# Optimization experiments

Measured on AMD Instinct MI355X. Metric: run time of the kernel, lower is better.

The kernel has to match this reference:

```python
import jax, jax.numpy as jnp
import numpy as np

N_NODES = 50000
N_EDGES = 800000
IN_DIM = 256
HID = [256, 128]
NEG_SLOPE = 0.01  # F.leaky_relu default


def setup_inputs() -> dict:
    key = jax.random.key(0)
    ks = jax.random.split(key, 8)
    x = jax.random.normal(ks[0], (N_NODES, IN_DIM), dtype=jnp.float32)
    w1 = jax.random.normal(ks[1], (IN_DIM, HID[0]), dtype=jnp.float32) * (1.0 / np.sqrt(IN_DIM))
    b1 = jnp.zeros((HID[0],), dtype=jnp.float32)
    w2 = jax.random.normal(ks[2], (HID[0], HID[1]), dtype=jnp.float32) * (1.0 / np.sqrt(HID[0]))
    b2 = jnp.zeros((HID[1],), dtype=jnp.float32)
    src = jax.random.randint(ks[3], (N_EDGES,), 0, N_NODES, dtype=jnp.int32)
    dst = jax.random.randint(ks[4], (N_EDGES,), 0, N_NODES, dtype=jnp.int32)
    edge_weight = jax.random.uniform(ks[5], (N_EDGES,), dtype=jnp.float32)
    return {"x": x, "w1": w1, "b1": b1, "w2": w2, "b2": b2,
            "src": src, "dst": dst, "edge_weight": edge_weight}


def _gcn_layer(h, w, b, src, dst, ew, n_nodes):
    # GraphConvolution: support = h @ W ; out = spmm(adj, support) + b
    support = h @ w                              # [N, d_out]
    msg = support[src] * ew[:, None]             # [E, d_out] gather + scale
    agg = jax.ops.segment_sum(msg, dst, num_segments=n_nodes)  # [N, d_out]
    return agg + b


def reference(x, w1, b1, w2, b2, src, dst, edge_weight):
    # layer 1: GCN -> leaky_relu -> dropout(eval: identity)
    h = _gcn_layer(x, w1, b1, src, dst, edge_weight, N_NODES)
    h = jax.nn.leaky_relu(h, NEG_SLOPE)
    # layer 2
    h = _gcn_layer(h, w2, b2, src, dst, edge_weight, N_NODES)
    h = jax.nn.leaky_relu(h, NEG_SLOPE)
    return h
```

## Files before the change

kernel.cpp:

```cpp
#include <hip/hip_runtime.h>

#define NEG_SLOPE 0.01f

constexpr int N_NODES_C = 50000;
constexpr int N_EDGES_C = 800000;
constexpr int M_PAD = 50048;

typedef short bf16x8 __attribute__((ext_vector_type(8)));
typedef float f32x4 __attribute__((ext_vector_type(4)));

__device__ inline unsigned short f2bf(float f) {
  unsigned int u = __float_as_uint(f);
  u += 0x7FFF + ((u >> 16) & 1);
  return (unsigned short)(u >> 16);
}
__device__ inline float bf2f(unsigned int h16) {
  return __uint_as_float(h16 << 16);
}

constexpr int NB_CONVX = (M_PAD * 32) / 256;
constexpr int NB_W1 = (256 * 256) / 256;
constexpr int NB_W2 = (256 * 128) / 256;
constexpr int NB_HIST = N_EDGES_C / 256;
constexpr int NB_PRE = NB_CONVX + NB_W1 + NB_W2 + NB_HIST;

__global__ __launch_bounds__(256) void pre_kernel(
    const float* __restrict__ x, const float* __restrict__ w1,
    const float* __restrict__ w2, const int* __restrict__ dst,
    unsigned short* __restrict__ xb, unsigned short* __restrict__ w1T,
    unsigned short* __restrict__ w2T, int* __restrict__ counts) {
  const int bx = blockIdx.x;
  const int tid = threadIdx.x;
  if (bx < NB_CONVX) {
    int idx = bx * 256 + tid;
    int row = idx >> 5;
    int c8 = (idx & 31) << 3;
    uint4 v;
    if (row < N_NODES_C) {
      const float4* p = (const float4*)(x + (size_t)row * 256 + c8);
      float4 a = p[0], b = p[1];
      v.x = f2bf(a.x) | ((unsigned)f2bf(a.y) << 16);
      v.y = f2bf(a.z) | ((unsigned)f2bf(a.w) << 16);
      v.z = f2bf(b.x) | ((unsigned)f2bf(b.y) << 16);
      v.w = f2bf(b.z) | ((unsigned)f2bf(b.w) << 16);
    } else {
      v = make_uint4(0, 0, 0, 0);
    }
    *(uint4*)(xb + (size_t)row * 256 + c8) = v;
  } else if (bx < NB_CONVX + NB_W1) {
    int idx = (bx - NB_CONVX) * 256 + tid;
    int n = idx >> 8, k = idx & 255;
    w1T[idx] = f2bf(w1[(size_t)k * 256 + n]);
  } else if (bx < NB_CONVX + NB_W1 + NB_W2) {
    int idx = (bx - NB_CONVX - NB_W1) * 256 + tid;
    int n = idx >> 8, k = idx & 255;
    w2T[idx] = f2bf(w2[(size_t)k * 128 + n]);
  } else {
    int e = (bx - NB_CONVX - NB_W1 - NB_W2) * 256 + tid;
    atomicAdd(&counts[dst[e]], 1);
  }
}

constexpr int N_SCAN_BLKS = (N_NODES_C + 255) / 256;

__global__ __launch_bounds__(256) void scan_phase_a(const int* __restrict__ counts,
                                                    int* __restrict__ partial,
                                                    int* __restrict__ blk_sums) {
  __shared__ int s[256];
  const int t = threadIdx.x;
  const int i = blockIdx.x * 256 + t;
  const int v = (i < N_NODES_C) ? counts[i] : 0;
  s[t] = v;
  __syncthreads();
  for (int off = 1; off < 256; off <<= 1) {
    int u = (t >= off) ? s[t - off] : 0;
    __syncthreads();
    s[t] += u;
    __syncthreads();
  }
  if (i < N_NODES_C) partial[i] = s[t] - v;
  if (t == 255) blk_sums[blockIdx.x] = s[255];
}

__global__ __launch_bounds__(256) void scan_phase_b(const int* __restrict__ blk_sums,
                                                    int* __restrict__ blk_off) {
  __shared__ int s[256];
  const int t = threadIdx.x;
  const int v = (t < N_SCAN_BLKS) ? blk_sums[t] : 0;
  s[t] = v;
  __syncthreads();
  for (int off = 1; off < 256; off <<= 1) {
    int u = (t >= off) ? s[t - off] : 0;
    __syncthreads();
    s[t] += u;
    __syncthreads();
  }
  if (t < N_SCAN_BLKS) blk_off[t] = s[t] - v;
}

__global__ __launch_bounds__(256) void scan_phase_c(const int* __restrict__ partial,
                                                    const int* __restrict__ blk_off,
                                                    int* __restrict__ row_ptr,
                                                    int* __restrict__ cursor) {
  const int i = blockIdx.x * 256 + threadIdx.x;
  if (i < N_NODES_C) {
    const int r = partial[i] + blk_off[blockIdx.x];
    row_ptr[i] = r;
    cursor[i] = r;
  }
  if (i == 0) row_ptr[N_NODES_C] = N_EDGES_C;
}

__global__ __launch_bounds__(256) void fill_kernel(const int* __restrict__ src,
                                                   const int* __restrict__ dst,
                                                   const float* __restrict__ ew,
                                                   int* __restrict__ cursor,
                                                   uint2* __restrict__ s_meta) {
  int e = blockIdx.x * 256 + threadIdx.x;
  if (e < N_EDGES_C) {
    int p = atomicAdd(&cursor[dst[e]], 1);
    uint2 m;
    m.x = (unsigned)src[e];
    m.y = __float_as_uint(ew[e]);
    s_meta[p] = m;
  }
}


#define GLOAD_LDS16(g, l)                                              \
  __builtin_amdgcn_global_load_lds(                                    \
      (__attribute__((address_space(1))) void*)(g),                    \
      (__attribute__((address_space(3))) void*)(l), 16, 0, 0)

__global__ __launch_bounds__(256) void gemm_bf16_kernel(
    const unsigned short* __restrict__ A,
    const unsigned short* __restrict__ BT,
    unsigned short* __restrict__ C,
    int N) {
  constexpr int K = 256;
  __shared__ short Asm[128 * 32];
  __shared__ short Bsm[128 * 32];
  const int tid = threadIdx.x;
  const int lane = tid & 63, wave = tid >> 6;
  const int wm = wave & 1, wn = wave >> 1;
  const int row0 = blockIdx.y * 128, col0 = blockIdx.x * 128;

  const int ch0 = wave * 2, ch1 = wave * 2 + 1;
  const int o0 = ch0 * 512 + lane * 8;
  const int o1 = ch1 * 512 + lane * 8;
  const int r0 = o0 >> 5, c0 = o0 & 31;
  const int r1 = o1 >> 5, c1 = o1 & 31;

  f32x4 acc[4][4] = {};

  for (int k0 = 0; k0 < K; k0 += 32) {
    GLOAD_LDS16(A + (size_t)(row0 + r0) * K + k0 + c0, &Asm[ch0 * 512]);
    GLOAD_LDS16(A + (size_t)(row0 + r1) * K + k0 + c1, &Asm[ch1 * 512]);
    GLOAD_LDS16(BT + (size_t)(col0 + r0) * K + k0 + c0, &Bsm[ch0 * 512]);
    GLOAD_LDS16(BT + (size_t)(col0 + r1) * K + k0 + c1, &Bsm[ch1 * 512]);
    __builtin_amdgcn_s_waitcnt(0);
    __syncthreads();

    bf16x8 af[4], bf[4];
#pragma unroll
    for (int mt = 0; mt < 4; ++mt)
      af[mt] = *(const bf16x8*)&Asm[(wm * 64 + mt * 16 + (lane & 15)) * 32 + (lane >> 4) * 8];
#pragma unroll
    for (int nt = 0; nt < 4; ++nt)
      bf[nt] = *(const bf16x8*)&Bsm[(wn * 64 + nt * 16 + (lane & 15)) * 32 + (lane >> 4) * 8];
#pragma unroll
    for (int mt = 0; mt < 4; ++mt)
#pragma unroll
      for (int nt = 0; nt < 4; ++nt)
        acc[mt][nt] = __builtin_amdgcn_mfma_f32_16x16x32_bf16(af[mt], bf[nt], acc[mt][nt], 0, 0, 0);
    __syncthreads();
  }

  const int cl = lane & 15, rq = (lane >> 4) * 4;
#pragma unroll
  for (int mt = 0; mt < 4; ++mt) {
    const int rbase = row0 + wm * 64 + mt * 16 + rq;
#pragma unroll
    for (int nt = 0; nt < 4; ++nt) {
      const int col = col0 + wn * 64 + nt * 16 + cl;
      const size_t sbase = ((size_t)(col >> 5) * M_PAD) * 32 + (col & 31);
#pragma unroll
      for (int i = 0; i < 4; ++i)
        C[sbase + (size_t)(rbase + i) * 32] = f2bf(acc[mt][nt][i]);
    }
  }
}


__device__ inline void fma8(float* acc, uint4 v, float wt) {
  acc[0] += bf2f(v.x & 0xffffu) * wt;
  acc[1] += bf2f(v.x >> 16) * wt;
  acc[2] += bf2f(v.y & 0xffffu) * wt;
  acc[3] += bf2f(v.y >> 16) * wt;
  acc[4] += bf2f(v.z & 0xffffu) * wt;
  acc[5] += bf2f(v.z >> 16) * wt;
  acc[6] += bf2f(v.w & 0xffffu) * wt;
  acc[7] += bf2f(v.w >> 16) * wt;
}

template <int NSLICE, int OUT_D, bool OUT_BF16>
__global__ __launch_bounds__(256) void agg_quad_kernel(
    const unsigned short* __restrict__ supS,
    const uint2* __restrict__ s_meta, const int* __restrict__ row_ptr,
    const float* __restrict__ bias, unsigned short* __restrict__ out_bf,
    float* __restrict__ out_f, int n_total) {
  const int bx = blockIdx.x;
  const int slice = bx & (NSLICE - 1);
  const int group = bx / NSLICE;
  const int tid = threadIdx.x;
  const int quad = tid >> 2;
  const int dimg = tid & 3;
  const int n = group * 64 + quad;
  if (n >= n_total) return;
  const bool valid = n < N_NODES_C;
  const unsigned short* tab = supS + (size_t)slice * M_PAD * 32;

  float acc[8] = {};
  if (valid) {
    int j = row_ptr[n];
    const int end = row_ptr[n + 1];
    for (; j + 2 <= end; j += 2) {
      uint2 m0 = s_meta[j];
      uint2 m1 = s_meta[j + 1];
      uint4 v0 = *(const uint4*)(tab + m0.x * 32 + dimg * 8);
      uint4 v1 = *(const uint4*)(tab + m1.x * 32 + dimg * 8);
      fma8(acc, v0, __uint_as_float(m0.y));
      fma8(acc, v1, __uint_as_float(m1.y));
    }
    if (j < end) {
      uint2 m0 = s_meta[j];
      uint4 v0 = *(const uint4*)(tab + m0.x * 32 + dimg * 8);
      fma8(acc, v0, __uint_as_float(m0.y));
    }
  }

  const int dbase = slice * 32 + dimg * 8;
  if (OUT_BF16) {
    unsigned short o[8];
#pragma unroll
    for (int j = 0; j < 8; ++j) {
      float v = acc[j] + bias[dbase + j];
      v = v >= 0.f ? v : NEG_SLOPE * v;
      o[j] = f2bf(v);
    }
    uint4 pk;
    pk.x = o[0] | ((unsigned)o[1] << 16);
    pk.y = o[2] | ((unsigned)o[3] << 16);
    pk.z = o[4] | ((unsigned)o[5] << 16);
    pk.w = o[6] | ((unsigned)o[7] << 16);
    *(uint4*)(out_bf + (size_t)n * OUT_D + dbase) = pk;
  } else if (valid) {
    float r[8];
#pragma unroll
    for (int j = 0; j < 8; ++j) {
      float v = acc[j] + bias[dbase + j];
      r[j] = v >= 0.f ? v : NEG_SLOPE * v;
    }
    *(float4*)(out_f + (size_t)n * OUT_D + dbase) = make_float4(r[0], r[1], r[2], r[3]);
    *(float4*)(out_f + (size_t)n * OUT_D + dbase + 4) = make_float4(r[4], r[5], r[6], r[7]);
  }
}


extern "C" void kernel_launch(void* const* d_in, const int* in_sizes, int n_in,
                              void* d_out, int out_size, void* d_ws, size_t ws_size,
                              hipStream_t stream) {
  const float* x  = (const float*)d_in[0];
  const float* w1 = (const float*)d_in[1];
  const float* b1 = (const float*)d_in[2];
  const float* w2 = (const float*)d_in[3];
  const float* b2 = (const float*)d_in[4];
  const int*   src = (const int*)d_in[5];
  const int*   dst = (const int*)d_in[6];
  const float* ew  = (const float*)d_in[7];
  float* out = (float*)d_out;

  unsigned short* xb   = (unsigned short*)d_ws;
  unsigned short* a2b  = xb + (size_t)M_PAD * 256;
  unsigned short* sup1 = a2b + (size_t)M_PAD * 256;
  unsigned short* sup2 = sup1 + (size_t)M_PAD * 256;
  unsigned short* w1T  = sup2 + (size_t)M_PAD * 128;
  unsigned short* w2T  = w1T + 256 * 256;
  int* counts  = (int*)(w2T + 128 * 256);
  int* cursor  = counts + N_NODES_C;
  int* row_ptr = cursor + N_NODES_C;
  int* partial = row_ptr + (N_NODES_C + 1);
  int* blk_sums= partial + N_NODES_C;
  int* blk_off = blk_sums + 256;
  uint2* s_meta = (uint2*)(blk_off + 256 + 2);

  const int EB = (N_EDGES_C + 255) / 256;

  hipMemsetAsync(counts, 0, N_NODES_C * sizeof(int), stream);
  pre_kernel<<<NB_PRE, 256, 0, stream>>>(x, w1, w2, dst, xb, w1T, w2T, counts);

  scan_phase_a<<<N_SCAN_BLKS, 256, 0, stream>>>(counts, partial, blk_sums);
  scan_phase_b<<<1, 256, 0, stream>>>(blk_sums, blk_off);
  scan_phase_c<<<N_SCAN_BLKS, 256, 0, stream>>>(partial, blk_off, row_ptr, cursor);
  fill_kernel<<<EB, 256, 0, stream>>>(src, dst, ew, cursor, s_meta);

  gemm_bf16_kernel<<<dim3(2, M_PAD / 128), 256, 0, stream>>>(xb, w1T, sup1, 256);
  {
    const int groups = M_PAD / 64;
    agg_quad_kernel<8, 256, true><<<groups * 8, 256, 0, stream>>>(
        sup1, s_meta, row_ptr, b1, a2b, nullptr, M_PAD);
  }

  gemm_bf16_kernel<<<dim3(1, M_PAD / 128), 256, 0, stream>>>(a2b, w2T, sup2, 128);
  {
    const int groups = (N_NODES_C + 63) / 64;
    agg_quad_kernel<4, 128, false><<<groups * 4, 256, 0, stream>>>(
        sup2, s_meta, row_ptr, b2, nullptr, out, N_NODES_C);
  }
}
```

Before: 332.1 us.

## Fuse scan phases, merge fill with GEMM1, pack edge metadata, shrink agg blocks

Merges scan phases b and c into one kernel, where each block redoes the small block-sum scan itself. Runs the edge-fill pass in the same launch as the first GEMM as extra blocks. Packs each edge's source index (16 bits) and bf16 edge weight into a single 32-bit word, halving metadata traffic. Aggregation now uses 64-thread blocks covering 16 nodes each. This cuts launch count and gather bandwidth, at the cost of bf16 rounding of edge weights and a 16-bit source index limit (the 50000 nodes fit).

```diff
diff --git a/kernel.cpp b/kernel.cpp
--- a/kernel.cpp
+++ b/kernel.cpp
@@ -82,9 +82,12 @@
   if (t == 255) blk_sums[blockIdx.x] = s[255];
 }
 
-__global__ __launch_bounds__(256) void scan_phase_b(const int* __restrict__ blk_sums,
-                                                    int* __restrict__ blk_off) {
+__global__ __launch_bounds__(256) void scan_phase_bc(const int* __restrict__ partial,
+                                                     const int* __restrict__ blk_sums,
+                                                     int* __restrict__ row_ptr,
+                                                     int* __restrict__ cursor) {
   __shared__ int s[256];
+  __shared__ int blk_excl;
   const int t = threadIdx.x;
   const int v = (t < N_SCAN_BLKS) ? blk_sums[t] : 0;
   s[t] = v;
@@ -95,35 +98,15 @@
     s[t] += u;
     __syncthreads();
   }
-  if (t < N_SCAN_BLKS) blk_off[t] = s[t] - v;
-}
-
-__global__ __launch_bounds__(256) void scan_phase_c(const int* __restrict__ partial,
-                                                    const int* __restrict__ blk_off,
-                                                    int* __restrict__ row_ptr,
-                                                    int* __restrict__ cursor) {
-  const int i = blockIdx.x * 256 + threadIdx.x;
+  if (t == (int)blockIdx.x) blk_excl = s[t] - v;
+  __syncthreads();
+  const int i = blockIdx.x * 256 + t;
   if (i < N_NODES_C) {
-    const int r = partial[i] + blk_off[blockIdx.x];
+    const int r = partial[i] + blk_excl;
     row_ptr[i] = r;
     cursor[i] = r;
   }
   if (i == 0) row_ptr[N_NODES_C] = N_EDGES_C;
-}
-
-__global__ __launch_bounds__(256) void fill_kernel(const int* __restrict__ src,
-                                                   const int* __restrict__ dst,
-                                                   const float* __restrict__ ew,
-                                                   int* __restrict__ cursor,
-                                                   uint2* __restrict__ s_meta) {
-  int e = blockIdx.x * 256 + threadIdx.x;
-  if (e < N_EDGES_C) {
-    int p = atomicAdd(&cursor[dst[e]], 1);
-    uint2 m;
-    m.x = (unsigned)src[e];
-    m.y = __float_as_uint(ew[e]);
-    s_meta[p] = m;
-  }
 }
 
 
@@ -132,18 +115,15 @@
       (__attribute__((address_space(1))) void*)(g),                    \
       (__attribute__((address_space(3))) void*)(l), 16, 0, 0)
 
-__global__ __launch_bounds__(256) void gemm_bf16_kernel(
+__device__ __forceinline__ void gemm_tile(
     const unsigned short* __restrict__ A,
     const unsigned short* __restrict__ BT,
     unsigned short* __restrict__ C,
-    int N) {
+    int N, int row0, int col0, short* Asm, short* Bsm) {
   constexpr int K = 256;
-  __shared__ short Asm[128 * 32];
-  __shared__ short Bsm[128 * 32];
   const int tid = threadIdx.x;
   const int lane = tid & 63, wave = tid >> 6;
   const int wm = wave & 1, wn = wave >> 1;
-  const int row0 = blockIdx.y * 128, col0 = blockIdx.x * 128;
 
   const int ch0 = wave * 2, ch1 = wave * 2 + 1;
   const int o0 = ch0 * 512 + lane * 8;
@@ -189,6 +169,36 @@
         C[sbase + (size_t)(rbase + i) * 32] = f2bf(acc[mt][nt][i]);
     }
   }
+}
+
+constexpr int NB_GEMM1 = 2 * (M_PAD / 128);
+constexpr int NB_FILL = (N_EDGES_C + 255) / 256;
+
+__global__ __launch_bounds__(256) void fill_gemm1_kernel(
+    const unsigned short* __restrict__ A, const unsigned short* __restrict__ BT,
+    unsigned short* __restrict__ C, const int* __restrict__ src,
+    const int* __restrict__ dst, const float* __restrict__ ew,
+    int* __restrict__ cursor, unsigned* __restrict__ s_meta) {
+  __shared__ short Asm[128 * 32];
+  __shared__ short Bsm[128 * 32];
+  const int b = blockIdx.x;
+  if (b < NB_GEMM1) {
+    gemm_tile(A, BT, C, 256, (b >> 1) * 128, (b & 1) * 128, Asm, Bsm);
+  } else {
+    int e = (b - NB_GEMM1) * 256 + threadIdx.x;
+    if (e < N_EDGES_C) {
+      int p = atomicAdd(&cursor[dst[e]], 1);
+      s_meta[p] = (unsigned)src[e] | ((unsigned)f2bf(ew[e]) << 16);
+    }
+  }
+}
+
+__global__ __launch_bounds__(256) void gemm2_kernel(
+    const unsigned short* __restrict__ A, const unsigned short* __restrict__ BT,
+    unsigned short* __restrict__ C) {
+  __shared__ short Asm[128 * 32];
+  __shared__ short Bsm[128 * 32];
+  gemm_tile(A, BT, C, 128, blockIdx.x * 128, 0, Asm, Bsm);
 }
 
 
@@ -204,18 +214,18 @@
 }
 
 template <int NSLICE, int OUT_D, bool OUT_BF16>
-__global__ __launch_bounds__(256) void agg_quad_kernel(
+__global__ __launch_bounds__(64) void agg_lite_kernel(
     const unsigned short* __restrict__ supS,
-    const uint2* __restrict__ s_meta, const int* __restrict__ row_ptr,
-    const float* __restrict__ bias, unsigned short* __restrict__ out_bf,
-    float* __restrict__ out_f, int n_total) {
+    const unsigned* __restrict__ s_meta,
+    const int* __restrict__ row_ptr, const float* __restrict__ bias,
+    unsigned short* __restrict__ out_bf, float* __restrict__ out_f, int n_total) {
   const int bx = blockIdx.x;
   const int slice = bx & (NSLICE - 1);
   const int group = bx / NSLICE;
-  const int tid = threadIdx.x;
-  const int quad = tid >> 2;
-  const int dimg = tid & 3;
-  const int n = group * 64 + quad;
+  const int lane = threadIdx.x;
+  const int quad = lane >> 2;
+  const int dimg = lane & 3;
+  const int n = group * 16 + quad;
   if (n >= n_total) return;
   const bool valid = n < N_NODES_C;
   const unsigned short* tab = supS + (size_t)slice * M_PAD * 32;
@@ -225,17 +235,17 @@
     int j = row_ptr[n];
     const int end = row_ptr[n + 1];
     for (; j + 2 <= end; j += 2) {
-      uint2 m0 = s_meta[j];
-      uint2 m1 = s_meta[j + 1];
-      uint4 v0 = *(const uint4*)(tab + m0.x * 32 + dimg * 8);
-      uint4 v1 = *(const uint4*)(tab + m1.x * 32 + dimg * 8);
-      fma8(acc, v0, __uint_as_float(m0.y));
-      fma8(acc, v1, __uint_as_float(m1.y));
+      unsigned m0 = s_meta[j];
+      unsigned m1 = s_meta[j + 1];
+      uint4 v0 = *(const uint4*)(tab + (m0 & 0xffffu) * 32 + dimg * 8);
+      uint4 v1 = *(const uint4*)(tab + (m1 & 0xffffu) * 32 + dimg * 8);
+      fma8(acc, v0, bf2f(m0 >> 16));
+      fma8(acc, v1, bf2f(m1 >> 16));
     }
     if (j < end) {
-      uint2 m0 = s_meta[j];
-      uint4 v0 = *(const uint4*)(tab + m0.x * 32 + dimg * 8);
-      fma8(acc, v0, __uint_as_float(m0.y));
+      unsigned m0 = s_meta[j];
+      uint4 v0 = *(const uint4*)(tab + (m0 & 0xffffu) * 32 + dimg * 8);
+      fma8(acc, v0, bf2f(m0 >> 16));
     }
   }
 
@@ -244,9 +254,13 @@
     unsigned short o[8];
 #pragma unroll
     for (int j = 0; j < 8; ++j) {
-      float v = acc[j] + bias[dbase + j];
-      v = v >= 0.f ? v : NEG_SLOPE * v;
-      o[j] = f2bf(v);
+      if (valid) {
+        float v = acc[j] + bias[dbase + j];
+        v = v >= 0.f ? v : NEG_SLOPE * v;
+        o[j] = f2bf(v);
+      } else {
+        o[j] = 0;
+      }
     }
     uint4 pk;
     pk.x = o[0] | ((unsigned)o[1] << 16);
@@ -291,30 +305,21 @@
   int* row_ptr = cursor + N_NODES_C;
   int* partial = row_ptr + (N_NODES_C + 1);
   int* blk_sums= partial + N_NODES_C;
-  int* blk_off = blk_sums + 256;
-  uint2* s_meta = (uint2*)(blk_off + 256 + 2);
-
-  const int EB = (N_EDGES_C + 255) / 256;
+  unsigned* s_meta = (unsigned*)(blk_sums + 256);
 
   hipMemsetAsync(counts, 0, N_NODES_C * sizeof(int), stream);
   pre_kernel<<<NB_PRE, 256, 0, stream>>>(x, w1, w2, dst, xb, w1T, w2T, counts);
 
   scan_phase_a<<<N_SCAN_BLKS, 256, 0, stream>>>(counts, partial, blk_sums);
-  scan_phase_b<<<1, 256, 0, stream>>>(blk_sums, blk_off);
-  scan_phase_c<<<N_SCAN_BLKS, 256, 0, stream>>>(partial, blk_off, row_ptr, cursor);
-  fill_kernel<<<EB, 256, 0, stream>>>(src, dst, ew, cursor, s_meta);
-
-  gemm_bf16_kernel<<<dim3(2, M_PAD / 128), 256, 0, stream>>>(xb, w1T, sup1, 256);
-  {
-    const int groups = M_PAD / 64;
-    agg_quad_kernel<8, 256, true><<<groups * 8, 256, 0, stream>>>(
-        sup1, s_meta, row_ptr, b1, a2b, nullptr, M_PAD);
-  }
-
-  gemm_bf16_kernel<<<dim3(1, M_PAD / 128), 256, 0, stream>>>(a2b, w2T, sup2, 128);
-  {
-    const int groups = (N_NODES_C + 63) / 64;
-    agg_quad_kernel<4, 128, false><<<groups * 4, 256, 0, stream>>>(
-        sup2, s_meta, row_ptr, b2, nullptr, out, N_NODES_C);
-  }
-}
+  scan_phase_bc<<<N_SCAN_BLKS, 256, 0, stream>>>(partial, blk_sums, row_ptr, cursor);
+
+  fill_gemm1_kernel<<<NB_GEMM1 + NB_FILL, 256, 0, stream>>>(
+      xb, w1T, sup1, src, dst, ew, cursor, s_meta);
+
+  agg_lite_kernel<8, 256, true><<<(M_PAD / 16) * 8, 64, 0, stream>>>(
+      sup1, s_meta, row_ptr, b1, a2b, nullptr, M_PAD);
+
+  gemm2_kernel<<<M_PAD / 128, 256, 0, stream>>>(a2b, w2T, sup2);
+  agg_lite_kernel<4, 128, false><<<(N_NODES_C / 16) * 4, 64, 0, stream>>>(
+      sup2, s_meta, row_ptr, b2, nullptr, out, N_NODES_C);
+}
```

Result: faster. 305.7 us (-8.0%).
